# Performance work log

Hardware: AMD Instinct MI355X
Metric: run time of the kernel (lower is better)

Reference implementation:

```python
import jax, jax.numpy as jnp
import numpy as np

B, TQ, TK, D, DV = 8, 2048, 2048, 1024, 1024  # units == TK


def setup_inputs() -> dict:
    key = jax.random.key(0)
    kq, kk, kv, kb = jax.random.split(key, 4)
    q = jax.random.normal(kq, (B, TQ, D), dtype=jnp.float32)
    k = jax.random.normal(kk, (B, D, TK), dtype=jnp.float32)
    v = jax.random.normal(kv, (B, TK, DV), dtype=jnp.float32)
    b = 0.1 * jax.random.normal(kb, (TK,), dtype=jnp.float32)  # bias over key axis (units,)
    return {"q": q, "k": k, "v": v, "b": b}


def reference(q, k, v, b):
    # scores[b,i,j] = tanh(q_i . k_j + b_j)   -- additive-style biased dot scores
    scores = jnp.tanh(jnp.einsum("bqd,bdk->bqk", q, k) + b)  # [B, TQ, TK]
    # softmax over the key axis (axis=1 of the unbatched [TQ,TK] scores)
    weights = jax.nn.softmax(scores, axis=-1)
    # weighted sum of values
    context = jnp.einsum("bqk,bkv->bqv", weights, v)  # [B, TQ, DV]
    return context
```

## Files before the change

### kernel.cpp

```cpp
#include <hip/hip_runtime.h>
#include <hip/hip_bf16.h>
#include <stdint.h>

#define B_  8
#define TQ_ 2048
#define TK_ 2048
#define D_  1024
#define DV_ 1024

typedef __attribute__((ext_vector_type(8))) short  short8;
typedef __attribute__((ext_vector_type(4))) float  floatx4;

__device__ __forceinline__ void async_copy16(const void* g, void* l) {
  __builtin_amdgcn_global_load_lds(
      (const __attribute__((address_space(1))) unsigned int*)g,
      (__attribute__((address_space(3))) unsigned int*)l,
      16, 0, 0);
}

__device__ __forceinline__ ushort f2bf(float f) {
  union { __hip_bfloat16 b; ushort u; } cv;
  cv.b = __float2bfloat16(f);
  return cv.u;
}

__device__ __forceinline__ float bf2f(ushort u) {
  union { ushort u; __hip_bfloat16 b; } cv;
  cv.u = u;
  return __bfloat162float(cv.b);
}

__device__ __forceinline__ void transpose_body(const float* __restrict__ in,
                                               ushort* __restrict__ out,
                                               int R, int C, int r0, int c0,
                                               float (*tile)[65]) {
  const int t = threadIdx.x;
  {
    const int row = t >> 4, col = (t & 15) * 4;
    #pragma unroll
    for (int ro = 0; ro < 4; ro++) {
      const float4 f = *(const float4*)&in[(size_t)(r0 + ro * 16 + row) * C + c0 + col];
      tile[ro * 16 + row][col + 0] = f.x;
      tile[ro * 16 + row][col + 1] = f.y;
      tile[ro * 16 + row][col + 2] = f.z;
      tile[ro * 16 + row][col + 3] = f.w;
    }
  }
  __syncthreads();
  {
    const int c = t >> 4, rg = (t & 15) * 4;
    #pragma unroll
    for (int ro = 0; ro < 4; ro++) {
      const int cc = ro * 16 + c;
      ushort4 o;
      o.x = f2bf(tile[rg + 0][cc]);
      o.y = f2bf(tile[rg + 1][cc]);
      o.z = f2bf(tile[rg + 2][cc]);
      o.w = f2bf(tile[rg + 3][cc]);
      *(ushort4*)&out[(size_t)(c0 + cc) * R + r0 + rg] = o;
    }
  }
}

__global__ void prep(const float* __restrict__ q, const float* __restrict__ k,
                     const float* __restrict__ v, ushort* __restrict__ qb,
                     ushort* __restrict__ ktb, ushort* __restrict__ vtb) {
  __shared__ float tile[64][65];
  const int task = blockIdx.z >> 3;
  const int z    = blockIdx.z & 7;
  if (task == 0) {
    const float4* in  = (const float4*)(q + (size_t)z * TQ_ * D_);
    ushort4*      oup = (ushort4*)(qb + (size_t)z * TQ_ * D_);
    const int i0 = (blockIdx.y * 32 + blockIdx.x) * 1024 + threadIdx.x;
    #pragma unroll
    for (int it = 0; it < 4; it++) {
      const int i = i0 + it * 256;
      float4 f = in[i];
      ushort4 o;
      o.x = f2bf(f.x); o.y = f2bf(f.y); o.z = f2bf(f.z); o.w = f2bf(f.w);
      oup[i] = o;
    }
  } else if (task == 1) {
    transpose_body(k + (size_t)z * D_ * TK_, ktb + (size_t)z * TK_ * D_,
                   D_, TK_, blockIdx.y * 64, blockIdx.x * 64, tile);
  } else {
    transpose_body(v + (size_t)z * TK_ * DV_, vtb + (size_t)z * DV_ * TK_,
                   TK_, DV_, blockIdx.x * 64, blockIdx.y * 64, tile);
  }
}


#define WG_BARRIER() do { asm volatile("" ::: "memory");        \
                          __builtin_amdgcn_s_barrier();         \
                          asm volatile("" ::: "memory"); } while (0)
#define VMCNT(n) asm volatile("s_waitcnt vmcnt(" #n ")" ::: "memory")

template <int KDIM>
__device__ __forceinline__ void gemm_core8(const ushort* __restrict__ Ap,
                                           const ushort* __restrict__ Bp,
                                           char* lds, int bm0, int bn0,
                                           floatx4 (&acc)[8][4]) {
  const int t    = threadIdx.x;
  const int lane = t & 63;
  const int w    = t >> 6;
  const int wm   = w >> 2, wn = w & 3;
  const int lc   = lane & 15, q = lane >> 4;
  const int offq = (q ^ ((lc >> 1) & 3)) * 16;
  constexpr int NT = KDIM / 64;

  const char* Abase = lds + (wm * 128 + lc) * 64 + offq;
  const char* Bbase = lds + 65536 + (wn * 64 + lc) * 64 + offq;

  const int srow = t >> 2;
  const int sch  = (t & 3) ^ ((t >> 3) & 3);
  const ushort* gA = Ap + (size_t)(bm0 + srow) * KDIM + sch * 8;
  const ushort* gB = Bp + (size_t)(bn0 + srow) * KDIM + sch * 8;

  auto stageA = [&](int buf, int kh, int kb) {
    char* d = lds + buf * 32768 + kh * 16384 + t * 16;
    async_copy16(gA + kb, d);
    async_copy16(gA + (size_t)128 * KDIM + kb, d + 8192);
  };
  auto stageB = [&](int buf, int kh, int kb) {
    char* d = lds + 65536 + buf * 32768 + kh * 16384 + t * 16;
    async_copy16(gB + kb, d);
    async_copy16(gB + (size_t)128 * KDIM + kb, d + 8192);
  };

  #pragma unroll
  for (int mi = 0; mi < 8; ++mi)
    #pragma unroll
    for (int ni = 0; ni < 4; ++ni)
      acc[mi][ni] = (floatx4){0.f, 0.f, 0.f, 0.f};

  stageB(0, 0, 0);   stageA(0, 0, 0);
  stageB(0, 1, 32);  stageA(0, 1, 32);
  stageB(1, 0, 64);  stageA(1, 0, 64);
  stageB(1, 1, 96);
  VMCNT(10);
  WG_BARRIER();

  int kA1 = 96, kB0 = 128, kA0 = 128, kB1 = 160;

  short8 a[4], b0[4], b1[4];
  #pragma unroll 2
  for (int tt = 0; tt < NT; ++tt) {
    const int cur = tt & 1, nxt = cur ^ 1;
    const char* A  = Abase + cur * 32768;
    const char* Bq = Bbase + cur * 32768;

    #pragma unroll
    for (int j = 0; j < 4; ++j) a[j]  = *(const short8*)(A + j * 1024);
    #pragma unroll
    for (int i = 0; i < 4; ++i) b0[i] = *(const short8*)(Bq + i * 1024);
    stageA(nxt, 1, kA1); kA1 += 64; if (kA1 >= KDIM) kA1 -= KDIM;
    WG_BARRIER();
    __builtin_amdgcn_s_setprio(1);
    #pragma unroll
    for (int j = 0; j < 4; ++j)
      #pragma unroll
      for (int i = 0; i < 4; ++i)
        acc[j][i] = __builtin_amdgcn_mfma_f32_16x16x32_bf16(a[j], b0[i], acc[j][i], 0, 0, 0);
    __builtin_amdgcn_s_setprio(0);
    WG_BARRIER();

    #pragma unroll
    for (int j = 0; j < 4; ++j) a[j] = *(const short8*)(A + 4096 + j * 1024);
    stageB(cur, 0, kB0); kB0 += 64; if (kB0 >= KDIM) kB0 -= KDIM;
    VMCNT(10);
    WG_BARRIER();
    __builtin_amdgcn_s_setprio(1);
    #pragma unroll
    for (int j = 0; j < 4; ++j)
      #pragma unroll
      for (int i = 0; i < 4; ++i)
        acc[4 + j][i] = __builtin_amdgcn_mfma_f32_16x16x32_bf16(a[j], b0[i], acc[4 + j][i], 0, 0, 0);
    __builtin_amdgcn_s_setprio(0);
    WG_BARRIER();

    #pragma unroll
    for (int j = 0; j < 4; ++j) a[j]  = *(const short8*)(A + 16384 + j * 1024);
    #pragma unroll
    for (int i = 0; i < 4; ++i) b1[i] = *(const short8*)(Bq + 16384 + i * 1024);
    stageA(cur, 0, kA0); kA0 += 64; if (kA0 >= KDIM) kA0 -= KDIM;
    WG_BARRIER();
    __builtin_amdgcn_s_setprio(1);
    #pragma unroll
    for (int j = 0; j < 4; ++j)
      #pragma unroll
      for (int i = 0; i < 4; ++i)
        acc[j][i] = __builtin_amdgcn_mfma_f32_16x16x32_bf16(a[j], b1[i], acc[j][i], 0, 0, 0);
    __builtin_amdgcn_s_setprio(0);
    WG_BARRIER();

    #pragma unroll
    for (int j = 0; j < 4; ++j) a[j] = *(const short8*)(A + 16384 + 4096 + j * 1024);
    stageB(cur, 1, kB1); kB1 += 64; if (kB1 >= KDIM) kB1 -= KDIM;
    VMCNT(8);
    WG_BARRIER();
    __builtin_amdgcn_s_setprio(1);
    #pragma unroll
    for (int j = 0; j < 4; ++j)
      #pragma unroll
      for (int i = 0; i < 4; ++i)
        acc[4 + j][i] = __builtin_amdgcn_mfma_f32_16x16x32_bf16(a[j], b1[i], acc[4 + j][i], 0, 0, 0);
    __builtin_amdgcn_s_setprio(0);
    WG_BARRIER();
  }
  VMCNT(0);
}

__device__ __forceinline__ void xcd_coords(int& bx, int& by, int& bz) {
  const int gx = gridDim.x, gy = gridDim.y;
  int lidx = blockIdx.x + gx * (blockIdx.y + gy * blockIdx.z);
  const int nwg = gx * gy * gridDim.z;
  lidx = (lidx & 7) * (nwg >> 3) + (lidx >> 3);
  bx = lidx % gx;
  const int byz = lidx / gx;
  by = byz % gy;
  bz = byz / gy;
}

__global__ __launch_bounds__(512, 2)
void gemm_qk(const ushort* __restrict__ Q, const ushort* __restrict__ Kt,
             const float* __restrict__ bias, ushort* __restrict__ P,
             float* __restrict__ lsum) {
  __shared__ short8 ldsv[8192];
  char* lds = (char*)ldsv;
  int bx, by, z;
  xcd_coords(bx, by, z);
  const int bm0 = by * 256;
  const int bn0 = bx * 256;

  floatx4 acc[8][4];
  gemm_core8<D_>(Q + (size_t)z * TQ_ * D_, Kt + (size_t)z * TK_ * D_,
                 lds, bm0, bn0, acc);

  const int lane = threadIdx.x & 63;
  const int w    = threadIdx.x >> 6;
  const int wm   = w >> 2, wn = w & 3;
  const int lc   = lane & 15, q = lane >> 4;
  ushort* Pb = P + (size_t)z * TQ_ * TK_;
  float*  lz = lsum + z * TQ_;

  #pragma unroll
  for (int mi = 0; mi < 8; ++mi) {
    const int grow = bm0 + wm * 128 + mi * 16 + (q << 2);
    float rs[4] = {0.f, 0.f, 0.f, 0.f};
    #pragma unroll
    for (int ni = 0; ni < 4; ++ni) {
      const int gcol = bn0 + wn * 64 + ni * 16 + lc;
      const float bj = bias[gcol];
      #pragma unroll
      for (int r = 0; r < 4; ++r) {
        float s = acc[mi][ni][r] + bj;
        float tnh = 1.f - 2.f / (__expf(2.f * s) + 1.f);
        float p   = __expf(tnh);
        ushort pu = f2bf(p);
        Pb[(size_t)(grow + r) * TK_ + gcol] = pu;
        rs[r] += bf2f(pu);
      }
    }
    #pragma unroll
    for (int r = 0; r < 4; ++r) {
      rs[r] += __shfl_xor(rs[r], 1, 64);
      rs[r] += __shfl_xor(rs[r], 2, 64);
      rs[r] += __shfl_xor(rs[r], 4, 64);
      rs[r] += __shfl_xor(rs[r], 8, 64);
    }
    if (lc == 0) {
      #pragma unroll
      for (int r = 0; r < 4; ++r) atomicAdd(&lz[grow + r], rs[r]);
    }
  }
}

__global__ __launch_bounds__(512, 2)
void gemm_pv(const ushort* __restrict__ P, const ushort* __restrict__ Vt,
             const float* __restrict__ lsum, float* __restrict__ out) {
  __shared__ short8 ldsv[8192];
  char* lds = (char*)ldsv;
  int bx, by, z;
  xcd_coords(bx, by, z);
  const int bm0 = by * 256;
  const int bn0 = bx * 256;

  floatx4 acc[8][4];
  gemm_core8<TK_>(P + (size_t)z * TQ_ * TK_, Vt + (size_t)z * DV_ * TK_,
                  lds, bm0, bn0, acc);

  const int lane = threadIdx.x & 63;
  const int w    = threadIdx.x >> 6;
  const int wm   = w >> 2, wn = w & 3;
  const int lc   = lane & 15, q = lane >> 4;
  float* ob = out + (size_t)z * TQ_ * DV_;
  const float* lz = lsum + z * TQ_;

  #pragma unroll
  for (int mi = 0; mi < 8; ++mi) {
    const int grow = bm0 + wm * 128 + mi * 16 + (q << 2);
    float linv[4];
    #pragma unroll
    for (int r = 0; r < 4; ++r) linv[r] = 1.f / lz[grow + r];
    #pragma unroll
    for (int ni = 0; ni < 4; ++ni) {
      const int gcol = bn0 + wn * 64 + ni * 16 + lc;
      #pragma unroll
      for (int r = 0; r < 4; ++r)
        ob[(size_t)(grow + r) * DV_ + gcol] = acc[mi][ni][r] * linv[r];
    }
  }
}


extern "C" void kernel_launch(void* const* d_in, const int* in_sizes, int n_in,
                              void* d_out, int out_size, void* d_ws, size_t ws_size,
                              hipStream_t stream) {
  const float* q    = (const float*)d_in[0];
  const float* k    = (const float*)d_in[1];
  const float* v    = (const float*)d_in[2];
  const float* bias = (const float*)d_in[3];
  float* out = (float*)d_out;

  char* ws = (char*)d_ws;
  ushort* qb   = (ushort*)(ws);
  ushort* ktb  = (ushort*)(ws + 33554432);
  ushort* vtb  = (ushort*)(ws + 67108864);
  ushort* P    = (ushort*)(ws + 100663296);
  float*  lsum = (float*)(ws + 167772160);

  hipMemsetAsync(lsum, 0, B_ * TQ_ * sizeof(float), stream);

  prep<<<dim3(32, 16, 24), dim3(256), 0, stream>>>(q, k, v, qb, ktb, vtb);

  gemm_qk<<<dim3(TK_ / 256, TQ_ / 256, B_), dim3(512), 0, stream>>>(qb, ktb, bias, P, lsum);
  gemm_pv<<<dim3(DV_ / 256, TQ_ / 256, B_), dim3(512), 0, stream>>>(P, vtb, lsum, out);
}
```

Baseline: 382.8 us.

## Software-pipeline LDS fragment reads in PV GEMM core with named LDS buffers

Adds a dedicated PV GEMM main loop that prefetches the next A/B fragments from LDS into a second register set while the MFMAs run on the current set, so LDS reads overlap with matrix math. The loop is unrolled over two K-tiles with separate named shared arrays, and it uses sched_barrier to pin instruction order. The result is one barrier per quarter-step instead of two. This costs more VGPRs for the extra fragment registers and relies on a delicate vmcnt/barrier ordering. The QK kernel is only renamed.

Measured after the change: 376.9 us. About the same (-1.5%).

```diff
diff --git a/kernel.cpp b/kernel.cpp
--- a/kernel.cpp
+++ b/kernel.cpp
@@ -90,16 +90,16 @@
 }
 
 
-#define WG_BARRIER() do { asm volatile("" ::: "memory");        \
-                          __builtin_amdgcn_s_barrier();         \
-                          asm volatile("" ::: "memory"); } while (0)
-#define VMCNT(n) asm volatile("s_waitcnt vmcnt(" #n ")" ::: "memory")
+#define WGB_Q() do { asm volatile("" ::: "memory");        \
+                     __builtin_amdgcn_s_barrier();         \
+                     asm volatile("" ::: "memory"); } while (0)
+#define VMC_Q(n) asm volatile("s_waitcnt vmcnt(" #n ")" ::: "memory")
 
 template <int KDIM>
-__device__ __forceinline__ void gemm_core8(const ushort* __restrict__ Ap,
-                                           const ushort* __restrict__ Bp,
-                                           char* lds, int bm0, int bn0,
-                                           floatx4 (&acc)[8][4]) {
+__device__ __forceinline__ void gemm_core_qk(const ushort* __restrict__ Ap,
+                                             const ushort* __restrict__ Bp,
+                                             char* lds, int bm0, int bn0,
+                                             floatx4 (&acc)[8][4]) {
   const int t    = threadIdx.x;
   const int lane = t & 63;
   const int w    = t >> 6;
@@ -137,8 +137,8 @@
   stageB(0, 1, 32);  stageA(0, 1, 32);
   stageB(1, 0, 64);  stageA(1, 0, 64);
   stageB(1, 1, 96);
-  VMCNT(10);
-  WG_BARRIER();
+  VMC_Q(10);
+  WGB_Q();
 
   int kA1 = 96, kB0 = 128, kA0 = 128, kB1 = 160;
 
@@ -154,7 +154,7 @@
     #pragma unroll
     for (int i = 0; i < 4; ++i) b0[i] = *(const short8*)(Bq + i * 1024);
     stageA(nxt, 1, kA1); kA1 += 64; if (kA1 >= KDIM) kA1 -= KDIM;
-    WG_BARRIER();
+    WGB_Q();
     __builtin_amdgcn_s_setprio(1);
     #pragma unroll
     for (int j = 0; j < 4; ++j)
@@ -162,13 +162,13 @@
       for (int i = 0; i < 4; ++i)
         acc[j][i] = __builtin_amdgcn_mfma_f32_16x16x32_bf16(a[j], b0[i], acc[j][i], 0, 0, 0);
     __builtin_amdgcn_s_setprio(0);
-    WG_BARRIER();
+    WGB_Q();
 
     #pragma unroll
     for (int j = 0; j < 4; ++j) a[j] = *(const short8*)(A + 4096 + j * 1024);
     stageB(cur, 0, kB0); kB0 += 64; if (kB0 >= KDIM) kB0 -= KDIM;
-    VMCNT(10);
-    WG_BARRIER();
+    VMC_Q(10);
+    WGB_Q();
     __builtin_amdgcn_s_setprio(1);
     #pragma unroll
     for (int j = 0; j < 4; ++j)
@@ -176,14 +176,14 @@
       for (int i = 0; i < 4; ++i)
         acc[4 + j][i] = __builtin_amdgcn_mfma_f32_16x16x32_bf16(a[j], b0[i], acc[4 + j][i], 0, 0, 0);
     __builtin_amdgcn_s_setprio(0);
-    WG_BARRIER();
+    WGB_Q();
 
     #pragma unroll
     for (int j = 0; j < 4; ++j) a[j]  = *(const short8*)(A + 16384 + j * 1024);
     #pragma unroll
     for (int i = 0; i < 4; ++i) b1[i] = *(const short8*)(Bq + 16384 + i * 1024);
     stageA(cur, 0, kA0); kA0 += 64; if (kA0 >= KDIM) kA0 -= KDIM;
-    WG_BARRIER();
+    WGB_Q();
     __builtin_amdgcn_s_setprio(1);
     #pragma unroll
     for (int j = 0; j < 4; ++j)
@@ -191,13 +191,13 @@
       for (int i = 0; i < 4; ++i)
         acc[j][i] = __builtin_amdgcn_mfma_f32_16x16x32_bf16(a[j], b1[i], acc[j][i], 0, 0, 0);
     __builtin_amdgcn_s_setprio(0);
-    WG_BARRIER();
+    WGB_Q();
 
     #pragma unroll
     for (int j = 0; j < 4; ++j) a[j] = *(const short8*)(A + 16384 + 4096 + j * 1024);
     stageB(cur, 1, kB1); kB1 += 64; if (kB1 >= KDIM) kB1 -= KDIM;
-    VMCNT(8);
-    WG_BARRIER();
+    VMC_Q(8);
+    WGB_Q();
     __builtin_amdgcn_s_setprio(1);
     #pragma unroll
     for (int j = 0; j < 4; ++j)
@@ -205,9 +205,118 @@
       for (int i = 0; i < 4; ++i)
         acc[4 + j][i] = __builtin_amdgcn_mfma_f32_16x16x32_bf16(a[j], b1[i], acc[4 + j][i], 0, 0, 0);
     __builtin_amdgcn_s_setprio(0);
-    WG_BARRIER();
-  }
-  VMCNT(0);
+    WGB_Q();
+  }
+  VMC_Q(0);
+}
+
+
+#define SB_F() __builtin_amdgcn_sched_barrier(0xF)
+#define PV_BAR() do { SB_F(); __builtin_amdgcn_s_barrier(); SB_F(); } while (0)
+
+#define STG(gsrc, kb, dstarr) do {                                         \
+    async_copy16((gsrc) + (kb), (char*)(dstarr) + t * 16);                 \
+    async_copy16((gsrc) + g2 + (kb), (char*)(dstarr) + 8192 + t * 16);     \
+  } while (0)
+
+#define RD4(dst, arr, extra)                                               \
+  _Pragma("unroll")                                                        \
+  for (int j = 0; j < 4; ++j)                                              \
+    dst[j] = *(const short8*)((const char*)(arr) + offA + (extra) + j * 1024);
+
+#define RDB(dst, arr)                                                      \
+  _Pragma("unroll")                                                        \
+  for (int i = 0; i < 4; ++i)                                              \
+    dst[i] = *(const short8*)((const char*)(arr) + offB + i * 1024);
+
+#define MM8(R, aset, bset)                                                 \
+  __builtin_amdgcn_s_setprio(1);                                           \
+  _Pragma("unroll")                                                        \
+  for (int j = 0; j < 4; ++j)                                              \
+    _Pragma("unroll")                                                      \
+    for (int i = 0; i < 4; ++i)                                            \
+      acc[(R) + j][i] = __builtin_amdgcn_mfma_f32_16x16x32_bf16(           \
+          aset[j], bset[i], acc[(R) + j][i], 0, 0, 0);                     \
+  __builtin_amdgcn_s_setprio(0);
+
+#define ROLLK(kv) do { kv += 64; if (kv >= KDIM) kv -= KDIM; } while (0)
+
+#define PV_TILE(AK0, AK1, BK0, BK1, ANK0, ANK1, BNK0) do {                 \
+                    \
+    PV_BAR();                                                              \
+    STG(gA, kA1, ANK1); ROLLK(kA1);                                        \
+    MM8(0, aX, b0);                                                        \
+    RD4(aY, AK0, 4096);                                                    \
+     \
+    PV_BAR();                                                              \
+    asm volatile("s_waitcnt vmcnt(8)");                                    \
+    STG(gB, kB0, BK0); ROLLK(kB0);                                         \
+    MM8(4, aY, b0);                                                        \
+    RD4(aX, AK1, 0);                                                       \
+    RDB(b1, BK1);                                                          \
+                    \
+    PV_BAR();                                                              \
+    STG(gA, kA0, AK0); ROLLK(kA0);                                         \
+    MM8(0, aX, b1);                                                        \
+    RD4(aY, AK1, 4096);                                                    \
+    \
+    PV_BAR();                                                              \
+    asm volatile("s_waitcnt vmcnt(6)");                                    \
+    STG(gB, kB1, BK1); ROLLK(kB1);                                         \
+    MM8(4, aY, b1);                                                        \
+    RD4(aX, ANK0, 0);                                                      \
+    RDB(b0, BNK0);                                                         \
+  } while (0)
+
+template <int KDIM>
+__device__ __forceinline__ void gemm_core_pv(const ushort* __restrict__ Ap,
+                                             const ushort* __restrict__ Bp,
+                                             int bm0, int bn0,
+                                             floatx4 (&acc)[8][4]) {
+  __shared__ short8 A0K0[1024], A0K1[1024], A1K0[1024], A1K1[1024];
+  __shared__ short8 B0K0[1024], B0K1[1024], B1K0[1024], B1K1[1024];
+
+  const int t    = threadIdx.x;
+  const int lane = t & 63;
+  const int w    = t >> 6;
+  const int wm   = w >> 2, wn = w & 3;
+  const int lc   = lane & 15, q = lane >> 4;
+  const int offq = (q ^ ((lc >> 1) & 3)) * 16;
+  const int offA = (wm * 128 + lc) * 64 + offq;
+  const int offB = (wn * 64  + lc) * 64 + offq;
+  constexpr int NT = KDIM / 64;
+
+  const int srow = t >> 2;
+  const int sch  = (t & 3) ^ ((t >> 3) & 3);
+  const ushort* gA = Ap + (size_t)(bm0 + srow) * KDIM + sch * 8;
+  const ushort* gB = Bp + (size_t)(bn0 + srow) * KDIM + sch * 8;
+  const size_t g2 = (size_t)128 * KDIM;
+
+  #pragma unroll
+  for (int mi = 0; mi < 8; ++mi)
+    #pragma unroll
+    for (int ni = 0; ni < 4; ++ni)
+      acc[mi][ni] = (floatx4){0.f, 0.f, 0.f, 0.f};
+
+  STG(gB, 0,  B0K0);  STG(gA, 0,  A0K0);
+  STG(gB, 32, B0K1);  STG(gA, 32, A0K1);
+  STG(gB, 64, B1K0);  STG(gA, 64, A1K0);
+  STG(gB, 96, B1K1);
+  asm volatile("s_waitcnt vmcnt(10)");
+  __builtin_amdgcn_s_barrier();
+  SB_F();
+
+  short8 aX[4], aY[4], b0[4], b1[4];
+  RD4(aX, A0K0, 0);
+  RDB(b0, B0K0);
+
+  int kA1 = 96, kB0 = 128, kA0 = 128, kB1 = 160;
+
+  for (int t2 = 0; t2 < NT / 2; ++t2) {
+    PV_TILE(A0K0, A0K1, B0K0, B0K1, A1K0, A1K1, B1K0);
+    PV_TILE(A1K0, A1K1, B1K0, B1K1, A0K0, A0K1, B0K0);
+  }
+  asm volatile("s_waitcnt vmcnt(0)");
 }
 
 __device__ __forceinline__ void xcd_coords(int& bx, int& by, int& bz) {
@@ -233,8 +342,8 @@
   const int bn0 = bx * 256;
 
   floatx4 acc[8][4];
-  gemm_core8<D_>(Q + (size_t)z * TQ_ * D_, Kt + (size_t)z * TK_ * D_,
-                 lds, bm0, bn0, acc);
+  gemm_core_qk<D_>(Q + (size_t)z * TQ_ * D_, Kt + (size_t)z * TK_ * D_,
+                   lds, bm0, bn0, acc);
 
   const int lane = threadIdx.x & 63;
   const int w    = threadIdx.x >> 6;
@@ -278,16 +387,14 @@
 __global__ __launch_bounds__(512, 2)
 void gemm_pv(const ushort* __restrict__ P, const ushort* __restrict__ Vt,
              const float* __restrict__ lsum, float* __restrict__ out) {
-  __shared__ short8 ldsv[8192];
-  char* lds = (char*)ldsv;
   int bx, by, z;
   xcd_coords(bx, by, z);
   const int bm0 = by * 256;
   const int bn0 = bx * 256;
 
   floatx4 acc[8][4];
-  gemm_core8<TK_>(P + (size_t)z * TQ_ * TK_, Vt + (size_t)z * DV_ * TK_,
-                  lds, bm0, bn0, acc);
+  gemm_core_pv<TK_>(P + (size_t)z * TQ_ * TK_, Vt + (size_t)z * DV_ * TK_,
+                    bm0, bn0, acc);
 
   const int lane = threadIdx.x & 63;
   const int w    = threadIdx.x >> 6;
```
